# Kernel tuning notes

Measured on AMD Instinct MI355X. Metric: run time of the kernel, lower is better.

Reference implementation:

```python
import jax, jax.numpy as jnp
import numpy as np

N_NODES = 15000
N_EDGES = 40000
N_GRAPHS = 750
D = 64
NODE_DIM = 32
EDGE_DIM = 16
NUM_CONV = 3
S2S_STEPS = 3


def setup_inputs() -> dict:
    key = jax.random.key(0)
    ks = jax.random.split(key, 24)
    s = 0.05
    inp = {
        'x': jax.random.normal(ks[0], (N_NODES, NODE_DIM), jnp.float32),
        'edge_attr': jax.random.uniform(ks[1], (N_EDGES, EDGE_DIM), jnp.float32),
        'edge_index': jax.random.randint(ks[2], (2, N_EDGES), 0, N_NODES),
        'batch': jnp.sort(jax.random.randint(ks[3], (N_NODES,), 0, N_GRAPHS)),
        # input projection
        'in_W': jax.random.normal(ks[4], (NODE_DIM, D)) * s,
        'in_b': jnp.zeros((D,)),
        # edge MLP -> per-edge DxD weights
        'e1_W': jax.random.normal(ks[5], (EDGE_DIM, D)) * s,
        'e1_b': jnp.zeros((D,)),
        'e2_W': jax.random.normal(ks[6], (D, D * D)) * s,
        'e2_b': jnp.zeros((D * D,)),
        'conv_b': jnp.zeros((D,)),
        # GRU (gate order r,z,n like torch)
        'gru_Wih': jax.random.normal(ks[7], (3 * D, D)) * s,
        'gru_Whh': jax.random.normal(ks[8], (3 * D, D)) * s,
        'gru_bih': jnp.zeros((3 * D,)),
        'gru_bhh': jnp.zeros((3 * D,)),
        # Set2Set LSTM (gate order i,f,g,o like torch), input 2D -> hidden D
        'lstm_Wih': jax.random.normal(ks[9], (4 * D, 2 * D)) * s,
        'lstm_Whh': jax.random.normal(ks[10], (4 * D, D)) * s,
        'lstm_bih': jnp.zeros((4 * D,)),
        'lstm_bhh': jnp.zeros((4 * D,)),
        # output MLP
        'out1_W': jax.random.normal(ks[11], (2 * D, 2 * D)) * s,
        'out1_b': jnp.zeros((2 * D,)),
        'out2_W': jax.random.normal(ks[12], (2 * D, 1)) * s,
        'out2_b': jnp.zeros((1,)),
    }
    return inp


def _gru_cell(m, h, Wih, Whh, bih, bhh):
    gi = m @ Wih.T + bih
    gh = h @ Whh.T + bhh
    ir, iz, inn = jnp.split(gi, 3, axis=-1)
    hr, hz, hn = jnp.split(gh, 3, axis=-1)
    r = jax.nn.sigmoid(ir + hr)
    z = jax.nn.sigmoid(iz + hz)
    n = jnp.tanh(inn + r * hn)
    return (1.0 - z) * n + z * h


def _lstm_cell(q, h, c, Wih, Whh, bih, bhh):
    g = q @ Wih.T + bih + h @ Whh.T + bhh
    i, f, gg, o = jnp.split(g, 4, axis=-1)
    c = jax.nn.sigmoid(f) * c + jax.nn.sigmoid(i) * jnp.tanh(gg)
    h = jax.nn.sigmoid(o) * jnp.tanh(c)
    return h, c


def reference(x, edge_attr, edge_index, batch,
              in_W, in_b, e1_W, e1_b, e2_W, e2_b, conv_b,
              gru_Wih, gru_Whh, gru_bih, gru_bhh,
              lstm_Wih, lstm_Whh, lstm_bih, lstm_bhh,
              out1_W, out1_b, out2_W, out2_b):
    src, dst = edge_index[0], edge_index[1]
    out = jax.nn.relu(x @ in_W + in_b)           # [N, D]
    h = out
    # edge-conditioned weights (edge_attr is constant across conv iters)
    W_e = (jax.nn.relu(edge_attr @ e1_W + e1_b) @ e2_W + e2_b).reshape(-1, D, D)  # [E, D, D]
    deg = jnp.maximum(jax.ops.segment_sum(jnp.ones((N_EDGES,), out.dtype), dst, N_NODES), 1.0)
    for _ in range(NUM_CONV):
        msg = jnp.einsum('ed,edf->ef', out[src], W_e)          # per-edge matmul
        agg = jax.ops.segment_sum(msg, dst, N_NODES) / deg[:, None]  # scatter-mean
        m = jax.nn.relu(agg + conv_b)
        h = _gru_cell(m, h, gru_Wih, gru_Whh, gru_bih, gru_bhh)
        out = h
    # Set2Set pooling
    q_star = jnp.zeros((N_GRAPHS, 2 * D), out.dtype)
    hl = jnp.zeros((N_GRAPHS, D), out.dtype)
    cl = jnp.zeros((N_GRAPHS, D), out.dtype)
    for _ in range(S2S_STEPS):
        hl, cl = _lstm_cell(q_star, hl, cl, lstm_Wih, lstm_Whh, lstm_bih, lstm_bhh)
        q = hl
        e = jnp.sum(out * q[batch], axis=-1)                    # [N]
        e = e - jax.ops.segment_max(e, batch, N_GRAPHS)[batch]
        ee = jnp.exp(e)
        a = ee / jax.ops.segment_sum(ee, batch, N_GRAPHS)[batch]
        r = jax.ops.segment_sum(a[:, None] * out, batch, N_GRAPHS)  # [G, D]
        q_star = jnp.concatenate([q, r], axis=-1)
    z = jax.nn.relu(q_star @ out1_W + out1_b) @ out2_W + out2_b
    return z
```

## Files before the change

kernel.cpp:

```cpp
#include <hip/hip_runtime.h>
#include <math.h>

#define N_NODES 15000
#define N_EDGES 40000
#define N_GRAPHS 750
#define N_TILES 938

typedef __attribute__((ext_vector_type(8))) short bf16x8;
typedef __attribute__((ext_vector_type(4))) float f32x4;

__device__ __forceinline__ float sigmoidf_(float x) { return 1.f / (1.f + expf(-x)); }

__device__ __forceinline__ unsigned short f2bf(float v) {
    unsigned u = __float_as_uint(v);
    unsigned r = (u + 0x7FFFu + ((u >> 16) & 1u)) >> 16;
    return (unsigned short)r;
}
__device__ __forceinline__ float bf2f(unsigned short b) {
    return __uint_as_float(((unsigned)b) << 16);
}

__global__ void count_kernel(const int* __restrict__ src, const int* __restrict__ dst,
                             int* __restrict__ tcnt, float* __restrict__ deg) {
    int e = blockIdx.x * 256 + threadIdx.x;
    if (e >= N_EDGES) return;
    atomicAdd(&tcnt[src[e] >> 4], 1);
    atomicAdd(&deg[dst[e]], 1.f);
}

__global__ void tscan_kernel(const int* __restrict__ tcnt, int* __restrict__ tptr,
                             int* __restrict__ cursor) {
    __shared__ int buf[1024];
    int t = threadIdx.x;
    int v = (t < N_TILES) ? tcnt[t] : 0;
    buf[t] = v;
    __syncthreads();
    for (int ofs = 1; ofs < 1024; ofs <<= 1) {
        int a = (t >= ofs) ? buf[t - ofs] : 0;
        __syncthreads();
        buf[t] += a;
        __syncthreads();
    }
    if (t < N_TILES) {
        int excl = buf[t] - v;
        tptr[t] = excl;
        cursor[t] = excl;
    }
    if (t == N_TILES - 1) tptr[N_TILES] = buf[t];
}

__global__ void fill_kernel(const int* __restrict__ src, int* __restrict__ cursor,
                            int* __restrict__ edge_list) {
    int e = blockIdx.x * 256 + threadIdx.x;
    if (e >= N_EDGES) return;
    int slot = atomicAdd(&cursor[src[e] >> 4], 1);
    edge_list[slot] = e;
}

__global__ __launch_bounds__(256)
void prep_kernel(const float* __restrict__ x, const float* __restrict__ in_W,
                 const float* __restrict__ in_b, float* __restrict__ node_h,
                 const float* __restrict__ e2b, float* __restrict__ Tb_g,
                 const float* __restrict__ ea, const float* __restrict__ e1_W,
                 const float* __restrict__ e1_b, float* __restrict__ h1,
                 const float* __restrict__ e2W,
                 unsigned short* __restrict__ Bhi, unsigned short* __restrict__ Blo,
                 const float* __restrict__ lWih, const float* __restrict__ lWhh,
                 const float* __restrict__ gWih, const float* __restrict__ gWhh,
                 float* __restrict__ lWihT, float* __restrict__ lWhhT,
                 unsigned short* __restrict__ gWihP, unsigned short* __restrict__ gWhhP,
                 unsigned short* __restrict__ e2bP,
                 const int* __restrict__ batch, int* __restrict__ gptr) {
    int b = blockIdx.x;
    int tid = threadIdx.x;
    if (b < 3750) {
        __shared__ float xs[4][32];
        __shared__ float hrow[4][64];
        int n0 = b * 4;
        if (tid < 128) xs[tid >> 5][tid & 31] = x[n0 * 32 + tid];
        __syncthreads();
        int nn = tid >> 6, f = tid & 63;
        float s = in_b[f];
        #pragma unroll
        for (int i = 0; i < 32; ++i) s += xs[nn][i] * in_W[i * 64 + f];
        s = fmaxf(s, 0.f);
        node_h[(size_t)(n0 + nn) * 64 + f] = s;
        hrow[nn][f] = s;
        __syncthreads();
        float t2 = 0.f;
        #pragma unroll 8
        for (int d = 0; d < 64; ++d) t2 += hrow[nn][d] * e2b[d * 64 + f];
        Tb_g[(size_t)(n0 + nn) * 64 + f] = t2;
    } else if (b < 13750) {
        __shared__ float eas[4][16];
        int e0 = (b - 3750) * 4;
        if (tid < 64) eas[tid >> 4][tid & 15] = ea[e0 * 16 + tid];
        __syncthreads();
        int nn = tid >> 6, f = tid & 63;
        float s = e1_b[f];
        #pragma unroll
        for (int i = 0; i < 16; ++i) s += eas[nn][i] * e1_W[i * 64 + f];
        h1[(size_t)(e0 + nn) * 64 + f] = fmaxf(s, 0.f);
    } else if (b < 14774) {
        int idx = (b - 13750) * 256 + tid;
        int j = idx & 7, lane = (idx >> 3) & 63, kt = (idx >> 9) & 1;
        int ct = (idx >> 10) & 31, ft = idx >> 15;
        int d = kt * 32 + ((lane >> 4) << 3) + j;
        int c = ct * 16 + (lane & 15);
        int kk = c >> 3, fi = c & 7;
        float v = e2W[(size_t)kk * 4096 + d * 64 + ft * 8 + fi];
        unsigned short hi = f2bf(v);
        Bhi[idx] = hi;
        Blo[idx] = f2bf(v - bf2f(hi));
    } else if (b < 14966) {
        int idx = (b - 14774) * 256 + tid;
        if (idx < 32768) {
            int i = idx >> 8, r = idx & 255;
            lWihT[i * 256 + r] = lWih[r * 128 + i];
        } else if (idx < 49152) {
            int x2 = idx - 32768; int i = x2 >> 8, r = x2 & 255;
            lWhhT[i * 256 + r] = lWhh[r * 64 + i];
        }
    } else if (b < 15078) {
        int idx = (b - 14966) * 256 + tid;
        if (idx < 12288) {
            int j = idx & 7, lane = (idx >> 3) & 63, kt = (idx >> 9) & 1, ct = idx >> 10;
            int k = kt * 32 + ((lane >> 4) << 3) + j;
            int n = ct * 16 + (lane & 15);
            float v = gWih[n * 64 + k];
            unsigned short hi = f2bf(v);
            gWihP[idx] = hi;
            gWihP[12288 + idx] = f2bf(v - bf2f(hi));
        } else if (idx < 24576) {
            int i2 = idx - 12288;
            int j = i2 & 7, lane = (i2 >> 3) & 63, kt = (i2 >> 9) & 1, ct = i2 >> 10;
            int k = kt * 32 + ((lane >> 4) << 3) + j;
            int n = ct * 16 + (lane & 15);
            float v = gWhh[n * 64 + k];
            unsigned short hi = f2bf(v);
            gWhhP[i2] = hi;
            gWhhP[12288 + i2] = f2bf(v - bf2f(hi));
        } else {
            int i2 = idx - 24576;
            int j = i2 & 7, lane = (i2 >> 3) & 63, kt = (i2 >> 9) & 1, ct = i2 >> 10;
            int k = kt * 32 + ((lane >> 4) << 3) + j;
            int n = ct * 16 + (lane & 15);
            float v = e2b[k * 64 + n];
            unsigned short hi = f2bf(v);
            e2bP[i2] = hi;
            e2bP[4096 + i2] = f2bf(v - bf2f(hi));
        }
    } else {
        int n = (b - 15078) * 256 + tid;
        if (n < N_NODES) {
            int bb = batch[n];
            int pb = (n == 0) ? -1 : batch[n - 1];
            for (int g = pb + 1; g <= bb; ++g) gptr[g] = n;
            if (n == N_NODES - 1)
                for (int g = bb + 1; g <= N_GRAPHS; ++g) gptr[g] = N_NODES;
        }
    }
}

__global__ __launch_bounds__(256, 4)
void conv_kernel(const float* __restrict__ node_h, const float* __restrict__ h1,
                 const unsigned short* __restrict__ Bhi, const unsigned short* __restrict__ Blo,
                 const float* __restrict__ Tb_g,
                 const int* __restrict__ tptr, const int* __restrict__ edge_list,
                 const int* __restrict__ src, const int* __restrict__ dst,
                 float* __restrict__ agg) {
    __shared__ float A_s[16][68];
    __shared__ float Tb_s[16][8];
    __shared__ float T_lds[16 * 552];
    int bid = blockIdx.x;
    int nt = bid >> 3, ft = bid & 7;
    int n0 = nt * 16;
    int tid = threadIdx.x;

    {
        int nn = tid >> 4, d4 = (tid & 15) * 4;
        int n = n0 + nn;
        float4 v = make_float4(0.f, 0.f, 0.f, 0.f);
        if (n < N_NODES) v = *(const float4*)(node_h + (size_t)n * 64 + d4);
        *(float4*)(&A_s[nn][d4]) = v;
    }
    if (tid < 128) {
        int nn = tid >> 3, fi = tid & 7;
        int n = n0 + nn;
        Tb_s[nn][fi] = (n < N_NODES) ? Tb_g[(size_t)n * 64 + ft * 8 + fi] : 0.f;
    }
    __syncthreads();

    int lane = tid & 63, wave = tid >> 6;
    int quad = lane >> 4, m = lane & 15;

    bf16x8 ahi[2], alo[2];
    #pragma unroll
    for (int kt = 0; kt < 2; ++kt) {
        const float* ap = &A_s[m][kt * 32 + quad * 8];
        float4 x0 = *(const float4*)ap;
        float4 x1 = *(const float4*)(ap + 4);
        float av[8] = {x0.x, x0.y, x0.z, x0.w, x1.x, x1.y, x1.z, x1.w};
        #pragma unroll
        for (int j = 0; j < 8; ++j) {
            unsigned short hi = f2bf(av[j]);
            ahi[kt][j] = (short)hi;
            alo[kt][j] = (short)f2bf(av[j] - bf2f(hi));
        }
    }

    size_t base0 = ((size_t)((ft * 32 + wave * 8) * 2) * 64 + lane) * 8;
    const unsigned short* ph = Bhi + base0;
    const unsigned short* pl = Blo + base0;
    bf16x8 bh0 = *(const bf16x8*)(ph);
    bf16x8 bh1 = *(const bf16x8*)(ph + 512);
    bf16x8 bl0 = *(const bf16x8*)(pl);
    bf16x8 bl1 = *(const bf16x8*)(pl + 512);

    #pragma unroll 1
    for (int ci = 0; ci < 8; ++ci) {
        bf16x8 ch0 = bh0, ch1 = bh1, cl0 = bl0, cl1 = bl1;
        if (ci < 7) {
            const unsigned short* nh = ph + (ci + 1) * 1024;
            const unsigned short* nl = pl + (ci + 1) * 1024;
            bh0 = *(const bf16x8*)(nh);
            bh1 = *(const bf16x8*)(nh + 512);
            bl0 = *(const bf16x8*)(nl);
            bl1 = *(const bf16x8*)(nl + 512);
        }
        f32x4 accA = {0.f, 0.f, 0.f, 0.f};
        f32x4 accB = {0.f, 0.f, 0.f, 0.f};
        accA = __builtin_amdgcn_mfma_f32_16x16x32_bf16(ahi[0], ch0, accA, 0, 0, 0);
        accB = __builtin_amdgcn_mfma_f32_16x16x32_bf16(ahi[1], ch1, accB, 0, 0, 0);
        accA = __builtin_amdgcn_mfma_f32_16x16x32_bf16(alo[0], ch0, accA, 0, 0, 0);
        accB = __builtin_amdgcn_mfma_f32_16x16x32_bf16(alo[1], ch1, accB, 0, 0, 0);
        accA = __builtin_amdgcn_mfma_f32_16x16x32_bf16(ahi[0], cl0, accA, 0, 0, 0);
        accB = __builtin_amdgcn_mfma_f32_16x16x32_bf16(ahi[1], cl1, accB, 0, 0, 0);
        int c = (wave * 8 + ci) * 16 + m;
        int kk = c >> 3, fi = c & 7;
        #pragma unroll
        for (int r = 0; r < 4; ++r)
            T_lds[(quad * 4 + r) * 552 + fi * 68 + kk] = accA[r] + accB[r];
    }
    __syncthreads();

    int fi = tid & 7, slot = tid >> 3;
    int te0 = tptr[nt], te1 = tptr[nt + 1];
    for (int c = te0 + slot; c < te1; c += 32) {
        int e = edge_list[c];
        int nn = src[e] - n0;
        const float* h1e = h1 + (size_t)e * 64;
        const float* Tr = &T_lds[nn * 552 + fi * 68];
        float s = Tb_s[nn][fi];
        #pragma unroll
        for (int k4 = 0; k4 < 64; k4 += 4) {
            float4 h4 = *(const float4*)(h1e + k4);
            float4 tv = *(const float4*)(Tr + k4);
            s += h4.x * tv.x + h4.y * tv.y + h4.z * tv.z + h4.w * tv.w;
        }
        atomicAdd(&agg[(size_t)dst[e] * 64 + ft * 8 + fi], s);
    }
}

__global__ __launch_bounds__(256, 2)
void gru_kernel(float* __restrict__ node_h, float* __restrict__ agg,
                const float* __restrict__ deg, const float* __restrict__ conv_b,
                const unsigned short* __restrict__ WihP, const unsigned short* __restrict__ WhhP,
                const float* __restrict__ bih, const float* __restrict__ bhh,
                const unsigned short* __restrict__ e2bP,
                float* __restrict__ Tb_g, int want_tb) {
    __shared__ unsigned short m_bf[2][64][72];
    __shared__ unsigned short h_bf[2][64][72];
    __shared__ unsigned short hn_bf[2][64][72];
    __shared__ float h_s[64][68];
    int n0 = blockIdx.x * 64;
    int tid = threadIdx.x;
    int lane = tid & 63, w = tid >> 6;
    int quad = lane >> 4, m16 = lane & 15;

    for (int i = tid; i < 4096; i += 256) {
        int c = i >> 6, f = i & 63;
        int n = n0 + c;
        float mv = 0.f, hv = 0.f;
        if (n < N_NODES) {
            float dg = fmaxf(deg[n], 1.f);
            mv = fmaxf(agg[(size_t)n * 64 + f] / dg + conv_b[f], 0.f);
            agg[(size_t)n * 64 + f] = 0.f;
            hv = node_h[(size_t)n * 64 + f];
        }
        unsigned short mh = f2bf(mv);
        m_bf[0][c][f] = mh; m_bf[1][c][f] = f2bf(mv - bf2f(mh));
        unsigned short hh = f2bf(hv);
        h_bf[0][c][f] = hh; h_bf[1][c][f] = f2bf(hv - bf2f(hh));
        h_s[c][f] = hv;
    }

    bf16x8 Bi[3][2][2], Bh[3][2][2];
    #pragma unroll
    for (int g = 0; g < 3; ++g)
        #pragma unroll
        for (int kt = 0; kt < 2; ++kt) {
            size_t base = ((size_t)((g * 4 + w) * 2 + kt) * 64 + lane) * 8;
            Bi[g][kt][0] = *(const bf16x8*)(WihP + base);
            Bi[g][kt][1] = *(const bf16x8*)(WihP + 12288 + base);
            Bh[g][kt][0] = *(const bf16x8*)(WhhP + base);
            Bh[g][kt][1] = *(const bf16x8*)(WhhP + 12288 + base);
        }
    int f = w * 16 + m16;
    float br_i = bih[f],       br_h = bhh[f];
    float bz_i = bih[64 + f],  bz_h = bhh[64 + f];
    float bn_i = bih[128 + f], bn_h = bhh[128 + f];
    __syncthreads();

    #pragma unroll 1
    for (int mt = 0; mt < 4; ++mt) {
        bf16x8 Am[2][2], Ah[2][2];
        #pragma unroll
        for (int kt = 0; kt < 2; ++kt) {
            Am[kt][0] = *(const bf16x8*)(&m_bf[0][mt * 16 + m16][kt * 32 + quad * 8]);
            Am[kt][1] = *(const bf16x8*)(&m_bf[1][mt * 16 + m16][kt * 32 + quad * 8]);
            Ah[kt][0] = *(const bf16x8*)(&h_bf[0][mt * 16 + m16][kt * 32 + quad * 8]);
            Ah[kt][1] = *(const bf16x8*)(&h_bf[1][mt * 16 + m16][kt * 32 + quad * 8]);
        }
        f32x4 ai[3], ah[3];
        #pragma unroll
        for (int g = 0; g < 3; ++g) { ai[g] = (f32x4){0.f,0.f,0.f,0.f}; ah[g] = (f32x4){0.f,0.f,0.f,0.f}; }
        #pragma unroll
        for (int g = 0; g < 3; ++g)
            #pragma unroll
            for (int kt = 0; kt < 2; ++kt) {
                ai[g] = __builtin_amdgcn_mfma_f32_16x16x32_bf16(Am[kt][0], Bi[g][kt][0], ai[g], 0, 0, 0);
                ai[g] = __builtin_amdgcn_mfma_f32_16x16x32_bf16(Am[kt][0], Bi[g][kt][1], ai[g], 0, 0, 0);
                ai[g] = __builtin_amdgcn_mfma_f32_16x16x32_bf16(Am[kt][1], Bi[g][kt][0], ai[g], 0, 0, 0);
                ah[g] = __builtin_amdgcn_mfma_f32_16x16x32_bf16(Ah[kt][0], Bh[g][kt][0], ah[g], 0, 0, 0);
                ah[g] = __builtin_amdgcn_mfma_f32_16x16x32_bf16(Ah[kt][0], Bh[g][kt][1], ah[g], 0, 0, 0);
                ah[g] = __builtin_amdgcn_mfma_f32_16x16x32_bf16(Ah[kt][1], Bh[g][kt][0], ah[g], 0, 0, 0);
            }
        #pragma unroll
        for (int r = 0; r < 4; ++r) {
            int node = mt * 16 + quad * 4 + r;
            float rr = sigmoidf_(ai[0][r] + br_i + ah[0][r] + br_h);
            float zz = sigmoidf_(ai[1][r] + bz_i + ah[1][r] + bz_h);
            float n2 = tanhf(ai[2][r] + bn_i + rr * (ah[2][r] + bn_h));
            float hnew = (1.f - zz) * n2 + zz * h_s[node][f];
            int n = n0 + node;
            if (n < N_NODES) node_h[(size_t)n * 64 + f] = hnew;
            unsigned short hh = f2bf(hnew);
            hn_bf[0][node][f] = hh;
            hn_bf[1][node][f] = f2bf(hnew - bf2f(hh));
        }
    }
    if (want_tb) {
        __syncthreads();
        bf16x8 Eb[2][2];
        #pragma unroll
        for (int kt = 0; kt < 2; ++kt) {
            size_t base = ((size_t)((w * 2 + kt) * 64) + lane) * 8;
            Eb[kt][0] = *(const bf16x8*)(e2bP + base);
            Eb[kt][1] = *(const bf16x8*)(e2bP + 4096 + base);
        }
        #pragma unroll 1
        for (int mt = 0; mt < 4; ++mt) {
            bf16x8 A2[2][2];
            #pragma unroll
            for (int kt = 0; kt < 2; ++kt) {
                A2[kt][0] = *(const bf16x8*)(&hn_bf[0][mt * 16 + m16][kt * 32 + quad * 8]);
                A2[kt][1] = *(const bf16x8*)(&hn_bf[1][mt * 16 + m16][kt * 32 + quad * 8]);
            }
            f32x4 acc = {0.f, 0.f, 0.f, 0.f};
            #pragma unroll
            for (int kt = 0; kt < 2; ++kt) {
                acc = __builtin_amdgcn_mfma_f32_16x16x32_bf16(A2[kt][0], Eb[kt][0], acc, 0, 0, 0);
                acc = __builtin_amdgcn_mfma_f32_16x16x32_bf16(A2[kt][0], Eb[kt][1], acc, 0, 0, 0);
                acc = __builtin_amdgcn_mfma_f32_16x16x32_bf16(A2[kt][1], Eb[kt][0], acc, 0, 0, 0);
            }
            #pragma unroll
            for (int r = 0; r < 4; ++r) {
                int n = n0 + mt * 16 + quad * 4 + r;
                if (n < N_NODES) Tb_g[(size_t)n * 64 + f] = acc[r];
            }
        }
    }
}

__global__ __launch_bounds__(128)
void s2s_kernel(const float* __restrict__ node_h, const int* __restrict__ gptr,
                const float* __restrict__ WihT, const float* __restrict__ WhhT,
                const float* __restrict__ bih, const float* __restrict__ bhh,
                const float* __restrict__ o1W, const float* __restrict__ o1b,
                const float* __restrict__ o2W, const float* __restrict__ o2b,
                float* __restrict__ z) {
    int g = blockIdx.x, tid = threadIdx.x;
    int f = tid & 63, half = tid >> 6;
    __shared__ float qs[128], hs[64], q[64], wts[128], gvs[4][64], racc_s[2][64];
    __shared__ float mred[2], sred[2], ored[2];
    if (half == 0) { qs[f] = 0.f; qs[64 + f] = 0.f; hs[f] = 0.f; }
    float c_t = 0.f;
    int nbeg = gptr[g], nend = gptr[g + 1];
    __syncthreads();
    for (int st = 0; st < 3; ++st) {
        #pragma unroll
        for (int gg = 0; gg < 2; ++gg) {
            int gate = half * 2 + gg;
            int row = gate * 64 + f;
            float s = bih[row] + bhh[row];
            #pragma unroll 8
            for (int i = 0; i < 128; ++i) s += qs[i] * WihT[i * 256 + row];
            #pragma unroll 8
            for (int i = 0; i < 64; ++i) s += hs[i] * WhhT[i * 256 + row];
            gvs[gate][f] = s;
        }
        __syncthreads();
        if (half == 0) {
            float c = sigmoidf_(gvs[1][f]) * c_t + sigmoidf_(gvs[0][f]) * tanhf(gvs[2][f]);
            float hn = sigmoidf_(gvs[3][f]) * tanhf(c);
            c_t = c;
            hs[f] = hn; q[f] = hn;
        }
        __syncthreads();
        float rm = -INFINITY, rs = 0.f, raccl = 0.f;
        for (int base = nbeg; base < nend; base += 128) {
            int n = base + tid;
            float e = -INFINITY;
            if (n < nend) {
                float s = 0.f;
                #pragma unroll 8
                for (int ff = 0; ff < 64; ++ff) s += node_h[(size_t)n * 64 + ff] * q[ff];
                e = s;
            }
            float cm = e;
            #pragma unroll
            for (int o = 32; o > 0; o >>= 1) cm = fmaxf(cm, __shfl_down(cm, o));
            if ((tid & 63) == 0) mred[half] = cm;
            __syncthreads();
            float bm = fmaxf(mred[0], mred[1]);
            float nm = fmaxf(rm, bm);
            float scale = (rm == -INFINITY) ? 0.f : expf(rm - nm);
            float wv = (n < nend) ? expf(e - nm) : 0.f;
            wts[tid] = wv;
            float cs = wv;
            #pragma unroll
            for (int o = 32; o > 0; o >>= 1) cs += __shfl_down(cs, o);
            if ((tid & 63) == 0) sred[half] = cs;
            __syncthreads();
            float bs = sred[0] + sred[1];
            float na = raccl * scale;
            int cnt2 = min(128, nend - base);
            int l0 = half * 64, l1 = min(l0 + 64, cnt2);
            for (int l = l0; l < l1; ++l) na += wts[l] * node_h[(size_t)(base + l) * 64 + f];
            raccl = na;
            rs = rs * scale + bs;
            rm = nm;
            __syncthreads();
        }
        racc_s[half][f] = raccl;
        __syncthreads();
        if (half == 0) {
            float r = (nend > nbeg) ? (racc_s[0][f] + racc_s[1][f]) / rs : 0.f;
            qs[f] = q[f];
            qs[64 + f] = r;
        }
        __syncthreads();
    }
    float sA = o1b[tid];
    #pragma unroll 8
    for (int i = 0; i < 128; ++i) sA += qs[i] * o1W[i * 128 + tid];
    float red = fmaxf(sA, 0.f) * o2W[tid];
    #pragma unroll
    for (int o = 32; o > 0; o >>= 1) red += __shfl_down(red, o);
    if ((tid & 63) == 0) ored[half] = red;
    __syncthreads();
    if (tid == 0) z[g] = ored[0] + ored[1] + o2b[0];
}

extern "C" void kernel_launch(void* const* d_in, const int* in_sizes, int n_in,
                              void* d_out, int out_size, void* d_ws, size_t ws_size,
                              hipStream_t stream) {
    const float* x         = (const float*)d_in[0];
    const float* edge_attr = (const float*)d_in[1];
    const int*   ei        = (const int*)d_in[2];
    const int*   batch     = (const int*)d_in[3];
    const float* in_W      = (const float*)d_in[4];
    const float* in_b      = (const float*)d_in[5];
    const float* e1_W      = (const float*)d_in[6];
    const float* e1_b      = (const float*)d_in[7];
    const float* e2_W      = (const float*)d_in[8];
    const float* e2_b      = (const float*)d_in[9];
    const float* conv_b    = (const float*)d_in[10];
    const float* gWih      = (const float*)d_in[11];
    const float* gWhh      = (const float*)d_in[12];
    const float* gbih      = (const float*)d_in[13];
    const float* gbhh      = (const float*)d_in[14];
    const float* lWih      = (const float*)d_in[15];
    const float* lWhh      = (const float*)d_in[16];
    const float* lbih      = (const float*)d_in[17];
    const float* lbhh      = (const float*)d_in[18];
    const float* o1W       = (const float*)d_in[19];
    const float* o1b       = (const float*)d_in[20];
    const float* o2W       = (const float*)d_in[21];
    const float* o2b       = (const float*)d_in[22];
    const int* src = ei;
    const int* dst = ei + N_EDGES;
    float* z = (float*)d_out;

    char* ws = (char*)d_ws;
    size_t off = 0;
    auto alloc = [&](size_t bytes) {
        void* p = ws + off;
        off = (off + bytes + 255) & ~(size_t)255;
        return p;
    };
    float* node_h   = (float*)alloc((size_t)N_NODES * 64 * 4);
    float* agg      = (float*)alloc((size_t)N_NODES * 64 * 4);
    float* h1       = (float*)alloc((size_t)N_EDGES * 64 * 4);
    unsigned short* Bhi = (unsigned short*)alloc((size_t)262144 * 2);
    unsigned short* Blo = (unsigned short*)alloc((size_t)262144 * 2);
    float* Tb_g     = (float*)alloc((size_t)N_NODES * 64 * 4);
    float* lWihT    = (float*)alloc(128 * 256 * 4);
    float* lWhhT    = (float*)alloc(64 * 256 * 4);
    unsigned short* gWihP = (unsigned short*)alloc(24576 * 2);
    unsigned short* gWhhP = (unsigned short*)alloc(24576 * 2);
    unsigned short* e2bP  = (unsigned short*)alloc(8192 * 2);
    float* deg      = (float*)alloc(N_NODES * 4);
    int*   tcnt     = (int*)alloc((N_TILES + 2) * 4);
    int*   tcursor  = (int*)alloc((N_TILES + 2) * 4);
    int*   tptr     = (int*)alloc((N_TILES + 1) * 4);
    int*   edge_list= (int*)alloc(N_EDGES * 4);
    int*   gptr     = (int*)alloc((N_GRAPHS + 1) * 4);

    size_t degpad = ((size_t)N_NODES * 4 + 255) & ~(size_t)255;
    hipMemsetAsync(deg, 0, degpad + (N_TILES + 2) * 4, stream);
    hipMemsetAsync(agg, 0, (size_t)N_NODES * 64 * 4, stream);

    count_kernel<<<(N_EDGES + 255) / 256, 256, 0, stream>>>(src, dst, tcnt, deg);
    tscan_kernel<<<1, 1024, 0, stream>>>(tcnt, tptr, tcursor);
    fill_kernel<<<(N_EDGES + 255) / 256, 256, 0, stream>>>(src, tcursor, edge_list);
    prep_kernel<<<15137, 256, 0, stream>>>(x, in_W, in_b, node_h, e2_b, Tb_g,
                                           edge_attr, e1_W, e1_b, h1,
                                           e2_W, Bhi, Blo,
                                           lWih, lWhh, gWih, gWhh,
                                           lWihT, lWhhT, gWihP, gWhhP, e2bP,
                                           batch, gptr);

    for (int it = 0; it < 3; ++it) {
        conv_kernel<<<N_TILES * 8, 256, 0, stream>>>(node_h, h1, Bhi, Blo, Tb_g,
                                                     tptr, edge_list, src, dst, agg);
        gru_kernel<<<235, 256, 0, stream>>>(node_h, agg, deg, conv_b,
                                            gWihP, gWhhP, gbih, gbhh,
                                            e2bP, Tb_g, (it < 2) ? 1 : 0);
    }
    s2s_kernel<<<N_GRAPHS, 128, 0, stream>>>(node_h, gptr, lWihT, lWhhT, lbih, lbhh,
                                             o1W, o1b, o2W, o2b, z);
}
```

Baseline: 456.0 us.

## Fuse edge counting into prep, reorder conv grid, halve GRU tile size

New measurement: 444.1 us. 1.03x faster.

```diff
diff --git a/kernel.cpp b/kernel.cpp
--- a/kernel.cpp
+++ b/kernel.cpp
@@ -5,6 +5,7 @@
 #define N_EDGES 40000
 #define N_GRAPHS 750
 #define N_TILES 938
+#define N_TILES_PAD 944
 
 typedef __attribute__((ext_vector_type(8))) short bf16x8;
 typedef __attribute__((ext_vector_type(4))) float f32x4;
@@ -18,14 +19,6 @@
 }
 __device__ __forceinline__ float bf2f(unsigned short b) {
     return __uint_as_float(((unsigned)b) << 16);
-}
-
-__global__ void count_kernel(const int* __restrict__ src, const int* __restrict__ dst,
-                             int* __restrict__ tcnt, float* __restrict__ deg) {
-    int e = blockIdx.x * 256 + threadIdx.x;
-    if (e >= N_EDGES) return;
-    atomicAdd(&tcnt[src[e] >> 4], 1);
-    atomicAdd(&deg[dst[e]], 1.f);
 }
 
 __global__ void tscan_kernel(const int* __restrict__ tcnt, int* __restrict__ tptr,
@@ -41,12 +34,9 @@
         buf[t] += a;
         __syncthreads();
     }
-    if (t < N_TILES) {
-        int excl = buf[t] - v;
-        tptr[t] = excl;
-        cursor[t] = excl;
-    }
-    if (t == N_TILES - 1) tptr[N_TILES] = buf[t];
+    int excl = buf[t] - v;
+    if (t <= N_TILES_PAD) tptr[t] = excl;
+    if (t < N_TILES) cursor[t] = excl;
 }
 
 __global__ void fill_kernel(const int* __restrict__ src, int* __restrict__ cursor,
@@ -70,7 +60,9 @@
                  float* __restrict__ lWihT, float* __restrict__ lWhhT,
                  unsigned short* __restrict__ gWihP, unsigned short* __restrict__ gWhhP,
                  unsigned short* __restrict__ e2bP,
-                 const int* __restrict__ batch, int* __restrict__ gptr) {
+                 const int* __restrict__ batch, int* __restrict__ gptr,
+                 const int* __restrict__ src, const int* __restrict__ dst,
+                 int* __restrict__ tcnt, float* __restrict__ deg) {
     int b = blockIdx.x;
     int tid = threadIdx.x;
     if (b < 3750) {
@@ -150,7 +142,7 @@
             e2bP[i2] = hi;
             e2bP[4096 + i2] = f2bf(v - bf2f(hi));
         }
-    } else {
+    } else if (b < 15137) {
         int n = (b - 15078) * 256 + tid;
         if (n < N_NODES) {
             int bb = batch[n];
@@ -158,6 +150,12 @@
             for (int g = pb + 1; g <= bb; ++g) gptr[g] = n;
             if (n == N_NODES - 1)
                 for (int g = bb + 1; g <= N_GRAPHS; ++g) gptr[g] = N_NODES;
+        }
+    } else {
+        int e = (b - 15137) * 256 + tid;
+        if (e < N_EDGES) {
+            atomicAdd(&tcnt[src[e] >> 4], 1);
+            atomicAdd(&deg[dst[e]], 1.f);
         }
     }
 }
@@ -171,9 +169,9 @@
                  float* __restrict__ agg) {
     __shared__ float A_s[16][68];
     __shared__ float Tb_s[16][8];
-    __shared__ float T_lds[16 * 552];
+    __shared__ float T_lds[16 * 548];
     int bid = blockIdx.x;
-    int nt = bid >> 3, ft = bid & 7;
+    int nt = bid % N_TILES_PAD, ft = bid / N_TILES_PAD;
     int n0 = nt * 16;
     int tid = threadIdx.x;
 
@@ -240,7 +238,7 @@
         int kk = c >> 3, fi = c & 7;
         #pragma unroll
         for (int r = 0; r < 4; ++r)
-            T_lds[(quad * 4 + r) * 552 + fi * 68 + kk] = accA[r] + accB[r];
+            T_lds[(quad * 4 + r) * 548 + fi * 68 + kk] = accA[r] + accB[r];
     }
     __syncthreads();
 
@@ -250,35 +248,45 @@
         int e = edge_list[c];
         int nn = src[e] - n0;
         const float* h1e = h1 + (size_t)e * 64;
-        const float* Tr = &T_lds[nn * 552 + fi * 68];
-        float s = Tb_s[nn][fi];
-        #pragma unroll
-        for (int k4 = 0; k4 < 64; k4 += 4) {
-            float4 h4 = *(const float4*)(h1e + k4);
-            float4 tv = *(const float4*)(Tr + k4);
-            s += h4.x * tv.x + h4.y * tv.y + h4.z * tv.z + h4.w * tv.w;
-        }
+        const float* Tr = &T_lds[nn * 548 + fi * 68];
+        float p0 = Tb_s[nn][fi], p1 = 0.f, p2 = 0.f, p3 = 0.f;
+        #pragma unroll
+        for (int k4 = 0; k4 < 64; k4 += 16) {
+            float4 ha = *(const float4*)(h1e + k4);
+            float4 ta = *(const float4*)(Tr + k4);
+            float4 hb = *(const float4*)(h1e + k4 + 4);
+            float4 tb = *(const float4*)(Tr + k4 + 4);
+            float4 hc = *(const float4*)(h1e + k4 + 8);
+            float4 tc = *(const float4*)(Tr + k4 + 8);
+            float4 hd = *(const float4*)(h1e + k4 + 12);
+            float4 td = *(const float4*)(Tr + k4 + 12);
+            p0 += ha.x * ta.x + ha.y * ta.y + ha.z * ta.z + ha.w * ta.w;
+            p1 += hb.x * tb.x + hb.y * tb.y + hb.z * tb.z + hb.w * tb.w;
+            p2 += hc.x * tc.x + hc.y * tc.y + hc.z * tc.z + hc.w * tc.w;
+            p3 += hd.x * td.x + hd.y * td.y + hd.z * td.z + hd.w * td.w;
+        }
+        float s = (p0 + p1) + (p2 + p3);
         atomicAdd(&agg[(size_t)dst[e] * 64 + ft * 8 + fi], s);
     }
 }
 
-__global__ __launch_bounds__(256, 2)
+__global__ __launch_bounds__(256, 4)
 void gru_kernel(float* __restrict__ node_h, float* __restrict__ agg,
                 const float* __restrict__ deg, const float* __restrict__ conv_b,
                 const unsigned short* __restrict__ WihP, const unsigned short* __restrict__ WhhP,
                 const float* __restrict__ bih, const float* __restrict__ bhh,
                 const unsigned short* __restrict__ e2bP,
                 float* __restrict__ Tb_g, int want_tb) {
-    __shared__ unsigned short m_bf[2][64][72];
-    __shared__ unsigned short h_bf[2][64][72];
-    __shared__ unsigned short hn_bf[2][64][72];
-    __shared__ float h_s[64][68];
-    int n0 = blockIdx.x * 64;
+    __shared__ unsigned short m_bf[2][32][72];
+    __shared__ unsigned short h_bf[2][32][72];
+    __shared__ unsigned short hn_bf[2][32][72];
+    __shared__ float h_s[32][68];
+    int n0 = blockIdx.x * 32;
     int tid = threadIdx.x;
     int lane = tid & 63, w = tid >> 6;
     int quad = lane >> 4, m16 = lane & 15;
 
-    for (int i = tid; i < 4096; i += 256) {
+    for (int i = tid; i < 2048; i += 256) {
         int c = i >> 6, f = i & 63;
         int n = n0 + c;
         float mv = 0.f, hv = 0.f;
@@ -313,7 +321,7 @@
     __syncthreads();
 
     #pragma unroll 1
-    for (int mt = 0; mt < 4; ++mt) {
+    for (int mt = 0; mt < 2; ++mt) {
         bf16x8 Am[2][2], Ah[2][2];
         #pragma unroll
         for (int kt = 0; kt < 2; ++kt) {
@@ -360,7 +368,7 @@
             Eb[kt][1] = *(const bf16x8*)(e2bP + 4096 + base);
         }
         #pragma unroll 1
-        for (int mt = 0; mt < 4; ++mt) {
+        for (int mt = 0; mt < 2; ++mt) {
             bf16x8 A2[2][2];
             #pragma unroll
             for (int kt = 0; kt < 2; ++kt) {
@@ -524,7 +532,7 @@
     float* deg      = (float*)alloc(N_NODES * 4);
     int*   tcnt     = (int*)alloc((N_TILES + 2) * 4);
     int*   tcursor  = (int*)alloc((N_TILES + 2) * 4);
-    int*   tptr     = (int*)alloc((N_TILES + 1) * 4);
+    int*   tptr     = (int*)alloc((N_TILES_PAD + 2) * 4);
     int*   edge_list= (int*)alloc(N_EDGES * 4);
     int*   gptr     = (int*)alloc((N_GRAPHS + 1) * 4);
 
@@ -532,20 +540,19 @@
     hipMemsetAsync(deg, 0, degpad + (N_TILES + 2) * 4, stream);
     hipMemsetAsync(agg, 0, (size_t)N_NODES * 64 * 4, stream);
 
-    count_kernel<<<(N_EDGES + 255) / 256, 256, 0, stream>>>(src, dst, tcnt, deg);
-    tscan_kernel<<<1, 1024, 0, stream>>>(tcnt, tptr, tcursor);
-    fill_kernel<<<(N_EDGES + 255) / 256, 256, 0, stream>>>(src, tcursor, edge_list);
-    prep_kernel<<<15137, 256, 0, stream>>>(x, in_W, in_b, node_h, e2_b, Tb_g,
+    prep_kernel<<<15294, 256, 0, stream>>>(x, in_W, in_b, node_h, e2_b, Tb_g,
                                            edge_attr, e1_W, e1_b, h1,
                                            e2_W, Bhi, Blo,
                                            lWih, lWhh, gWih, gWhh,
                                            lWihT, lWhhT, gWihP, gWhhP, e2bP,
-                                           batch, gptr);
+                                           batch, gptr, src, dst, tcnt, deg);
+    tscan_kernel<<<1, 1024, 0, stream>>>(tcnt, tptr, tcursor);
+    fill_kernel<<<(N_EDGES + 255) / 256, 256, 0, stream>>>(src, tcursor, edge_list);
 
     for (int it = 0; it < 3; ++it) {
-        conv_kernel<<<N_TILES * 8, 256, 0, stream>>>(node_h, h1, Bhi, Blo, Tb_g,
-                                                     tptr, edge_list, src, dst, agg);
-        gru_kernel<<<235, 256, 0, stream>>>(node_h, agg, deg, conv_b,
+        conv_kernel<<<N_TILES_PAD * 8, 256, 0, stream>>>(node_h, h1, Bhi, Blo, Tb_g,
+                                                         tptr, edge_list, src, dst, agg);
+        gru_kernel<<<469, 256, 0, stream>>>(node_h, agg, deg, conv_b,
                                             gWihP, gWhhP, gbih, gbhh,
                                             e2bP, Tb_g, (it < 2) ? 1 : 0);
     }
```
